# Performance work log

Hardware: AMD Instinct MI355X
Metric: run time of the kernel (lower is better)

The kernel has to match this reference:

```python
import jax, jax.numpy as jnp
import numpy as np

NEG_INF = -9e15


def setup_inputs() -> dict:
    key = jax.random.key(0)
    k1, k2, k3, k4 = jax.random.split(key, 4)
    N, F_in, H, F_out = 4096, 512, 8, 64
    node_features = jax.random.normal(k1, (N, F_in), dtype=jnp.float32)
    adj_matrix = jax.random.randint(k2, (N, N), 0, 2, dtype=jnp.int32)
    # ensure self-loops so every row has at least one unmasked entry
    adj_matrix = jnp.maximum(adj_matrix, jnp.eye(N, dtype=jnp.int32))
    W = jax.random.normal(k3, (H, F_in, F_out), dtype=jnp.float32) * 0.05
    a = jax.random.normal(k4, (H, 2 * F_out), dtype=jnp.float32) * 0.05
    return {"node_features": node_features, "adj_matrix": adj_matrix, "W": W, "a": a}


def reference(node_features, adj_matrix, W, a):
    alpha = 0.2
    H, F_in, F_out = W.shape
    # Per-head linear projection: [H, N, F_out]
    Wh = jnp.einsum("nf,hfo->hno", node_features, W)
    # Attention logits e_ij = LeakyReLU(a1 . Wh_i + a2 . Wh_j)
    f_src = jnp.einsum("hno,ho->hn", Wh, a[:, :F_out])   # [H, N]
    f_dst = jnp.einsum("hno,ho->hn", Wh, a[:, F_out:])   # [H, N]
    e = jax.nn.leaky_relu(f_src[:, :, None] + f_dst[:, None, :], negative_slope=alpha)  # [H, N, N]
    # Mask by adjacency, softmax over neighbors
    masked = jnp.where(adj_matrix[None, :, :] > 0, e, NEG_INF)
    attn = jax.nn.softmax(masked, axis=-1)               # [H, N, N]
    # Aggregate neighbor features per head
    h_prime = jnp.einsum("hnm,hmo->hno", attn, Wh)       # [H, N, F_out]
    # Concat heads along feature dim -> [N, H*F_out]
    return jnp.transpose(h_prime, (1, 0, 2)).reshape(h_prime.shape[1], H * F_out)
```

## Files before the change

kernel.cpp:

```cpp
#include <hip/hip_runtime.h>
#include <stdint.h>


#define NN 4096
#define FIN 512
#define NH 8
#define FO 64

typedef _Float16 f16x8 __attribute__((ext_vector_type(8)));
typedef _Float16 f16x2 __attribute__((ext_vector_type(2)));
typedef __attribute__((ext_vector_type(4))) float f32x4;

union H8 { f16x8 v; f16x2 p[4]; unsigned u[4]; };
union U2 { unsigned u; f16x2 v; };

#define GLOAD_LDS16(g, l)                                                          \
  __builtin_amdgcn_global_load_lds((__attribute__((address_space(1))) const void*)(g), \
                                   (__attribute__((address_space(3))) void*)(l), 16, 0, 0)
#define GLOAD_LDS4(g, l)                                                           \
  __builtin_amdgcn_global_load_lds((__attribute__((address_space(1))) const void*)(g), \
                                   (__attribute__((address_space(3))) void*)(l), 4, 0, 0)

__device__ __forceinline__ unsigned short f2h(float f) {
  _Float16 h = (_Float16)f;
  return __builtin_bit_cast(unsigned short, h);
}

__global__ __launch_bounds__(256) void prep_kernel(
    const float* __restrict__ X, const int* __restrict__ adj, const float* __restrict__ W,
    const float* __restrict__ a,
    unsigned short* __restrict__ Xh, unsigned short* __restrict__ WbT,
    unsigned* __restrict__ adjbitsT, unsigned short* __restrict__ WAh) {
  int bid = blockIdx.x, tid = threadIdx.x;
  if (bid < 2048) {
    int item = bid * 256 + tid;
    int jt = item >> 12, r = item & 4095;
    const int* p = adj + (size_t)r * NN + jt * 32;
    unsigned bits = 0;
#pragma unroll
    for (int b = 0; b < 32; b += 4) {
      int4 v = *(const int4*)(p + b);
      bits |= (unsigned)(v.x & 1) << b;
      bits |= (unsigned)(v.y & 1) << (b + 1);
      bits |= (unsigned)(v.z & 1) << (b + 2);
      bits |= (unsigned)(v.w & 1) << (b + 3);
    }
    adjbitsT[item] = bits;
  } else if (bid < 4096) {
    int item = (bid - 2048) * 256 + tid;
    float4 v = ((const float4*)X)[item];
    ushort4 o;
    o.x = f2h(v.x); o.y = f2h(v.y); o.z = f2h(v.z); o.w = f2h(v.w);
    ((ushort4*)Xh)[item] = o;
  } else if (bid < 5120) {
    int item = (bid - 4096) * 256 + tid;
    int o = item & 63, k = (item >> 6) & 511, h = item >> 15;
    WbT[h * 32768 + o * 512 + k] = f2h(W[h * 32768 + k * 64 + o]);
  } else {
    int item = (bid - 5120) * 256 + tid;
    int h = item >> 10, which = (item >> 9) & 1, k = item & 511;
    const float4* wp = (const float4*)(W + ((size_t)h * FIN + k) * FO);
    const float4* ap = (const float4*)(a + h * 128 + which * 64);
    float s = 0.f;
#pragma unroll
    for (int o4 = 0; o4 < 16; ++o4) {
      float4 w4 = wp[o4], a4 = ap[o4];
      s += w4.x * a4.x + w4.y * a4.y + w4.z * a4.z + w4.w * a4.w;
    }
    WAh[(h * 2 + which) * FIN + k] = f2h(s);
  }
}

__global__ __launch_bounds__(512, 4) void proj_sd_kernel(
    const unsigned short* __restrict__ Xh, const unsigned short* __restrict__ WbT,
    const unsigned short* __restrict__ WAh,
    unsigned short* __restrict__ Whfrag, float* __restrict__ Rf,
    unsigned short* __restrict__ E1h, unsigned short* __restrict__ E2h) {
  __shared__ float red[4 * 64 * 20];
  int lane = threadIdx.x & 63, wave = threadIdx.x >> 6;
  int row16 = lane & 15, grp = lane >> 4;
  int bx = blockIdx.x;
  if (bx >= 512) {
    int i0 = ((bx - 512) * 8 + wave) * 16;
    if (i0 >= NN) return;
    f32x4 acc = {0, 0, 0, 0};
    const unsigned short* xb = Xh + (size_t)(i0 + row16) * FIN + grp * 8;
    const unsigned short* wb = WAh + row16 * FIN + grp * 8;
#pragma unroll
    for (int k0 = 0; k0 < FIN; k0 += 32)
      acc = __builtin_amdgcn_mfma_f32_16x16x32_f16(*(const f16x8*)(xb + k0),
                                                   *(const f16x8*)(wb + k0), acc, 0, 0, 0);
    int hh = row16 >> 1;
#pragma unroll
    for (int reg = 0; reg < 4; ++reg) {
      int rr = i0 + grp * 4 + reg;
      float v = acc[reg];
      if (row16 & 1) {
        E1h[hh * NN + rr] = f2h(0.5f * __expf(v));
        E2h[hh * NN + rr] = f2h(0.5f * __expf(0.2f * v));
      } else {
        Rf[hh * NN + rr] = __expf(-0.8f * v);
      }
    }
    return;
  }
  int kh = wave >> 2, jb = wave & 3;
  int job = bx * 4 + jb;
  int h = job & 7, rt = job >> 3;
  int i0 = rt * 16;
  f32x4 acc[4] = {{0,0,0,0},{0,0,0,0},{0,0,0,0},{0,0,0,0}};
  const unsigned short* xb = Xh + (size_t)(i0 + row16) * FIN + kh * 256 + grp * 8;
  const unsigned short* wb = WbT + h * (FO * FIN) + row16 * FIN + kh * 256 + grp * 8;
#pragma unroll
  for (int k0 = 0; k0 < 256; k0 += 32) {
    f16x8 af = *(const f16x8*)(xb + k0);
#pragma unroll
    for (int cb = 0; cb < 4; ++cb)
      acc[cb] = __builtin_amdgcn_mfma_f32_16x16x32_f16(
          af, *(const f16x8*)(wb + cb * 16 * FIN + k0), acc[cb], 0, 0, 0);
  }
  if (kh == 1) {
    float* q = red + (jb * 64 + lane) * 20;
#pragma unroll
    for (int cb = 0; cb < 4; ++cb) *(f32x4*)(q + cb * 4) = acc[cb];
  }
  __syncthreads();
  if (kh == 0) {
    const float* q = red + (jb * 64 + lane) * 20;
#pragma unroll
    for (int cb = 0; cb < 4; ++cb) acc[cb] += *(const f32x4*)(q + cb * 4);
    int jt = i0 >> 5;
    int kk0 = (i0 & 31) + grp * 4;
    int tl = (kk0 >> 3) * 16 + row16;
    int e0 = kk0 & 7;
#pragma unroll
    for (int cb = 0; cb < 4; ++cb) {
      ushort4 pk;
      pk.x = f2h(acc[cb][0]); pk.y = f2h(acc[cb][1]);
      pk.z = f2h(acc[cb][2]); pk.w = f2h(acc[cb][3]);
      *(ushort4*)(Whfrag + (((size_t)h * 128 + jt) * 4 + cb) * 512 + tl * 8 + e0) = pk;
    }
  }
}

#define SEGB 4608
#define E_OFF 4096
#define A_OFF 4224

__global__ __launch_bounds__(256, 3) void gat_kernel(
    const unsigned* __restrict__ adjbitsT, const unsigned short* __restrict__ Whfrag,
    const float* __restrict__ Rf, const unsigned short* __restrict__ E1h,
    const unsigned short* __restrict__ E2h,
    float* __restrict__ N0, float* __restrict__ outbuf, float* __restrict__ Dd) {
  __shared__ __align__(16) char lds[36864];
  int h = blockIdx.y, z = blockIdx.z;
  int lane = threadIdx.x & 63, jseg = threadIdx.x >> 6;
  int row16 = lane & 15, grp = lane >> 4;
  int r0 = blockIdx.x * 64;
  int jt0 = z * 64 + jseg * 16;

  f16x2 Rh[4];
#pragma unroll
  for (int gi = 0; gi < 4; ++gi) {
    _Float16 rv = (_Float16)Rf[h * NN + r0 + gi * 16 + row16];
    Rh[gi][0] = rv; Rh[gi][1] = rv;
  }

  H8 ones;
#pragma unroll
  for (int k = 0; k < 4; ++k) ones.u[k] = 0x3C003C00u;

  const unsigned short* wsrc = Whfrag + (size_t)h * 262144 + (size_t)jt0 * 2048 + lane * 8;
  const unsigned short* esrc =
      ((lane & 4) ? E2h : E1h) + h * NN + jt0 * 32 + (lane & 3) * 8;
  const unsigned* asrc = adjbitsT + (size_t)jt0 * NN + r0 + lane;

  f32x4 acc[4][5];
#pragma unroll
  for (int gi = 0; gi < 4; ++gi)
#pragma unroll
    for (int cc = 0; cc < 5; ++cc) acc[gi][cc] = (f32x4){0, 0, 0, 0};

  char* seg0 = lds + (jseg * 2 + 0) * SEGB;
  char* seg1 = lds + (jseg * 2 + 1) * SEGB;

  auto stage = [&](char* seg, int p) {
    const unsigned short* bs = wsrc + (size_t)p * 2048;
    GLOAD_LDS16(bs, seg);
    GLOAD_LDS16(bs + 512, seg + 1024);
    GLOAD_LDS16(bs + 1024, seg + 2048);
    GLOAD_LDS16(bs + 1536, seg + 3072);
    GLOAD_LDS4(asrc + (size_t)p * NN, seg + A_OFF);
    if (lane < 8) GLOAD_LDS16(esrc + p * 32, seg + E_OFF);
  };

  auto compute = [&](const char* seg) {
    H8 e1, e2;
    e1.v = *(const f16x8*)(seg + E_OFF + grp * 16);
    e2.v = *(const f16x8*)(seg + E_OFF + 64 + grp * 16);
    const char* bp = seg + lane * 16;
    f16x8 b0 = *(const f16x8*)(bp);
    f16x8 b1 = *(const f16x8*)(bp + 1024);
    f16x8 b2 = *(const f16x8*)(bp + 2048);
    f16x8 b3 = *(const f16x8*)(bp + 3072);
#pragma unroll
    for (int gi = 0; gi < 4; ++gi) {
      unsigned bw = *(const unsigned*)(seg + A_OFF + (gi * 16 + row16) * 4);
      unsigned bb = (bw >> (grp * 8)) & 0xffu;
      unsigned t = bb | (bb << 15);
      H8 af;
#pragma unroll
      for (int k = 0; k < 4; ++k) {
        f16x2 mx = __builtin_elementwise_max(e1.p[k], Rh[gi] * e2.p[k]);
        U2 m;
        m.u = (t << (14 - 2 * k)) & 0x40004000u;
        af.p[k] = mx * m.v;
      }
      acc[gi][0] = __builtin_amdgcn_mfma_f32_16x16x32_f16(af.v, b0, acc[gi][0], 0, 0, 0);
      acc[gi][1] = __builtin_amdgcn_mfma_f32_16x16x32_f16(af.v, b1, acc[gi][1], 0, 0, 0);
      acc[gi][2] = __builtin_amdgcn_mfma_f32_16x16x32_f16(af.v, b2, acc[gi][2], 0, 0, 0);
      acc[gi][3] = __builtin_amdgcn_mfma_f32_16x16x32_f16(af.v, b3, acc[gi][3], 0, 0, 0);
      acc[gi][4] = __builtin_amdgcn_mfma_f32_16x16x32_f16(af.v, ones.v, acc[gi][4], 0, 0, 0);
    }
  };

  stage(seg0, 0);
  __syncthreads();
#pragma unroll 1
  for (int p2 = 0; p2 < 8; ++p2) {
    stage(seg1, 2 * p2 + 1);
    compute(seg0);
    __syncthreads();
    if (p2 < 7) stage(seg0, 2 * p2 + 2);
    compute(seg1);
    __syncthreads();
  }

  float* red = (float*)lds;
#pragma unroll
  for (int cc = 0; cc < 5; ++cc) {
    if (jseg != 0) {
#pragma unroll
      for (int gi = 0; gi < 4; ++gi)
        *(f32x4*)(red + (((jseg - 1) * 4 + gi) * 64 + lane) * 4) = acc[gi][cc];
    }
    __syncthreads();
    if (jseg == 0) {
#pragma unroll
      for (int s = 0; s < 3; ++s)
#pragma unroll
        for (int gi = 0; gi < 4; ++gi)
          acc[gi][cc] += *(const f32x4*)(red + ((s * 4 + gi) * 64 + lane) * 4);
    }
    __syncthreads();
  }

  if (jseg == 0) {
    float* base;
    int rs;
    if (z == 0) { base = N0 + (size_t)h * NN * FO; rs = FO; }
    else        { base = outbuf + h * FO;          rs = NH * FO; }
#pragma unroll
    for (int gi = 0; gi < 4; ++gi) {
#pragma unroll
      for (int reg = 0; reg < 4; ++reg) {
        int row = r0 + gi * 16 + grp * 4 + reg;
        float* op = base + (size_t)row * rs + row16;
        op[0]  = acc[gi][0][reg];
        op[16] = acc[gi][1][reg];
        op[32] = acc[gi][2][reg];
        op[48] = acc[gi][3][reg];
      }
      if (row16 == 0) {
#pragma unroll
        for (int reg = 0; reg < 4; ++reg)
          Dd[((size_t)z * NH + h) * NN + r0 + gi * 16 + grp * 4 + reg] = acc[gi][4][reg];
      }
    }
  }
}

__global__ __launch_bounds__(256) void norm_kernel(
    const float* __restrict__ N0, const float* __restrict__ Dd, float* __restrict__ out) {
  int idx = (blockIdx.x * 256 + threadIdx.x) * 4;
  int r = idx >> 9, c = idx & 511, h = c >> 6, o = c & 63;
  float4 n1 = *(const float4*)(out + idx);
  float4 n0 = *(const float4*)(N0 + ((size_t)h * NN + r) * FO + o);
  float inv = 1.0f / (Dd[h * NN + r] + Dd[(NH + h) * NN + r]);
  float4 res;
  res.x = (n1.x + n0.x) * inv;
  res.y = (n1.y + n0.y) * inv;
  res.z = (n1.z + n0.z) * inv;
  res.w = (n1.w + n0.w) * inv;
  *(float4*)(out + idx) = res;
}

extern "C" void kernel_launch(void* const* d_in, const int* in_sizes, int n_in,
                              void* d_out, int out_size, void* d_ws, size_t ws_size,
                              hipStream_t stream) {
  const float* X  = (const float*)d_in[0];
  const int* adj  = (const int*)d_in[1];
  const float* W  = (const float*)d_in[2];
  const float* a  = (const float*)d_in[3];
  float* out = (float*)d_out;
  char* ws = (char*)d_ws;

  unsigned short* Xh     = (unsigned short*)(ws + 0);
  unsigned short* WbT    = (unsigned short*)(ws + 4194304);
  unsigned* adjbitsT     = (unsigned*)(ws + 4718592);
  unsigned short* Whfrag = (unsigned short*)(ws + 6815744);
  unsigned short* WAh    = (unsigned short*)(ws + 11010048);
  float* Rf              = (float*)(ws + 11026432);
  unsigned short* E1h    = (unsigned short*)(ws + 11288576);
  unsigned short* E2h    = (unsigned short*)(ws + 11354112);
  float* N0              = (float*)(ws + 11534336);
  float* Dd              = (float*)(ws + 19922944);

  prep_kernel<<<5152, 256, 0, stream>>>(X, adj, W, a, Xh, WbT, adjbitsT, WAh);
  proj_sd_kernel<<<544, 512, 0, stream>>>(Xh, WbT, WAh, Whfrag, Rf, E1h, E2h);
  gat_kernel<<<dim3(64, 8, 2), 256, 0, stream>>>(adjbitsT, Whfrag, Rf, E1h, E2h, N0, out, Dd);
  norm_kernel<<<2048, 256, 0, stream>>>(N0, Dd, out);
}
```

Measured before the change: 86.80 us.

## Fuse X fp16 conversion into projection and drop split-K norm kernel

The separate X-to-fp16 pass in the prep kernel is removed; the projection kernel now loads fp32 X and converts it in registers. The attention kernel no longer splits the neighbor dimension across two z-blocks. Each block walks all 4096 columns and divides by the softmax denominator in its epilogue, which removes the N0/Dd intermediates and the norm kernel. The trade-off is half as many attention blocks (512 instead of 1024), so there is less parallelism and a longer serial loop per block, while X is read twice as fp32 by the projection.

Result: faster. 84.96 us (-2.1%).

```diff
diff --git a/kernel.cpp b/kernel.cpp
--- a/kernel.cpp
+++ b/kernel.cpp
@@ -26,11 +26,18 @@
   return __builtin_bit_cast(unsigned short, h);
 }
 
+__device__ __forceinline__ f16x8 ld_cvt8(const float* p) {
+  float4 a = *(const float4*)p, b = *(const float4*)(p + 4);
+  f16x8 r;
+  r[0] = (_Float16)a.x; r[1] = (_Float16)a.y; r[2] = (_Float16)a.z; r[3] = (_Float16)a.w;
+  r[4] = (_Float16)b.x; r[5] = (_Float16)b.y; r[6] = (_Float16)b.z; r[7] = (_Float16)b.w;
+  return r;
+}
+
 __global__ __launch_bounds__(256) void prep_kernel(
-    const float* __restrict__ X, const int* __restrict__ adj, const float* __restrict__ W,
-    const float* __restrict__ a,
-    unsigned short* __restrict__ Xh, unsigned short* __restrict__ WbT,
-    unsigned* __restrict__ adjbitsT, unsigned short* __restrict__ WAh) {
+    const int* __restrict__ adj, const float* __restrict__ W, const float* __restrict__ a,
+    unsigned short* __restrict__ WbT, unsigned* __restrict__ adjbitsT,
+    unsigned short* __restrict__ WAh) {
   int bid = blockIdx.x, tid = threadIdx.x;
   if (bid < 2048) {
     int item = bid * 256 + tid;
@@ -46,18 +53,12 @@
       bits |= (unsigned)(v.w & 1) << (b + 3);
     }
     adjbitsT[item] = bits;
-  } else if (bid < 4096) {
+  } else if (bid < 3072) {
     int item = (bid - 2048) * 256 + tid;
-    float4 v = ((const float4*)X)[item];
-    ushort4 o;
-    o.x = f2h(v.x); o.y = f2h(v.y); o.z = f2h(v.z); o.w = f2h(v.w);
-    ((ushort4*)Xh)[item] = o;
-  } else if (bid < 5120) {
-    int item = (bid - 4096) * 256 + tid;
     int o = item & 63, k = (item >> 6) & 511, h = item >> 15;
     WbT[h * 32768 + o * 512 + k] = f2h(W[h * 32768 + k * 64 + o]);
   } else {
-    int item = (bid - 5120) * 256 + tid;
+    int item = (bid - 3072) * 256 + tid;
     int h = item >> 10, which = (item >> 9) & 1, k = item & 511;
     const float4* wp = (const float4*)(W + ((size_t)h * FIN + k) * FO);
     const float4* ap = (const float4*)(a + h * 128 + which * 64);
@@ -72,7 +73,7 @@
 }
 
 __global__ __launch_bounds__(512, 4) void proj_sd_kernel(
-    const unsigned short* __restrict__ Xh, const unsigned short* __restrict__ WbT,
+    const float* __restrict__ X, const unsigned short* __restrict__ WbT,
     const unsigned short* __restrict__ WAh,
     unsigned short* __restrict__ Whfrag, float* __restrict__ Rf,
     unsigned short* __restrict__ E1h, unsigned short* __restrict__ E2h) {
@@ -84,11 +85,11 @@
     int i0 = ((bx - 512) * 8 + wave) * 16;
     if (i0 >= NN) return;
     f32x4 acc = {0, 0, 0, 0};
-    const unsigned short* xb = Xh + (size_t)(i0 + row16) * FIN + grp * 8;
+    const float* xb = X + (size_t)(i0 + row16) * FIN + grp * 8;
     const unsigned short* wb = WAh + row16 * FIN + grp * 8;
 #pragma unroll
     for (int k0 = 0; k0 < FIN; k0 += 32)
-      acc = __builtin_amdgcn_mfma_f32_16x16x32_f16(*(const f16x8*)(xb + k0),
+      acc = __builtin_amdgcn_mfma_f32_16x16x32_f16(ld_cvt8(xb + k0),
                                                    *(const f16x8*)(wb + k0), acc, 0, 0, 0);
     int hh = row16 >> 1;
 #pragma unroll
@@ -109,11 +110,11 @@
   int h = job & 7, rt = job >> 3;
   int i0 = rt * 16;
   f32x4 acc[4] = {{0,0,0,0},{0,0,0,0},{0,0,0,0},{0,0,0,0}};
-  const unsigned short* xb = Xh + (size_t)(i0 + row16) * FIN + kh * 256 + grp * 8;
+  const float* xb = X + (size_t)(i0 + row16) * FIN + kh * 256 + grp * 8;
   const unsigned short* wb = WbT + h * (FO * FIN) + row16 * FIN + kh * 256 + grp * 8;
 #pragma unroll
   for (int k0 = 0; k0 < 256; k0 += 32) {
-    f16x8 af = *(const f16x8*)(xb + k0);
+    f16x8 af = ld_cvt8(xb + k0);
 #pragma unroll
     for (int cb = 0; cb < 4; ++cb)
       acc[cb] = __builtin_amdgcn_mfma_f32_16x16x32_f16(
@@ -150,14 +151,13 @@
 __global__ __launch_bounds__(256, 3) void gat_kernel(
     const unsigned* __restrict__ adjbitsT, const unsigned short* __restrict__ Whfrag,
     const float* __restrict__ Rf, const unsigned short* __restrict__ E1h,
-    const unsigned short* __restrict__ E2h,
-    float* __restrict__ N0, float* __restrict__ outbuf, float* __restrict__ Dd) {
+    const unsigned short* __restrict__ E2h, float* __restrict__ out) {
   __shared__ __align__(16) char lds[36864];
-  int h = blockIdx.y, z = blockIdx.z;
+  int h = blockIdx.y;
   int lane = threadIdx.x & 63, jseg = threadIdx.x >> 6;
   int row16 = lane & 15, grp = lane >> 4;
   int r0 = blockIdx.x * 64;
-  int jt0 = z * 64 + jseg * 16;
+  int jt0 = jseg * 32;
 
   f16x2 Rh[4];
 #pragma unroll
@@ -227,11 +227,11 @@
   stage(seg0, 0);
   __syncthreads();
 #pragma unroll 1
-  for (int p2 = 0; p2 < 8; ++p2) {
+  for (int p2 = 0; p2 < 16; ++p2) {
     stage(seg1, 2 * p2 + 1);
     compute(seg0);
     __syncthreads();
-    if (p2 < 7) stage(seg0, 2 * p2 + 2);
+    if (p2 < 15) stage(seg0, 2 * p2 + 2);
     compute(seg1);
     __syncthreads();
   }
@@ -256,43 +256,20 @@
   }
 
   if (jseg == 0) {
-    float* base;
-    int rs;
-    if (z == 0) { base = N0 + (size_t)h * NN * FO; rs = FO; }
-    else        { base = outbuf + h * FO;          rs = NH * FO; }
 #pragma unroll
     for (int gi = 0; gi < 4; ++gi) {
 #pragma unroll
       for (int reg = 0; reg < 4; ++reg) {
+        float inv = 1.0f / acc[gi][4][reg];
         int row = r0 + gi * 16 + grp * 4 + reg;
-        float* op = base + (size_t)row * rs + row16;
-        op[0]  = acc[gi][0][reg];
-        op[16] = acc[gi][1][reg];
-        op[32] = acc[gi][2][reg];
-        op[48] = acc[gi][3][reg];
+        float* op = out + (size_t)row * (NH * FO) + h * FO + row16;
+        op[0]  = acc[gi][0][reg] * inv;
+        op[16] = acc[gi][1][reg] * inv;
+        op[32] = acc[gi][2][reg] * inv;
+        op[48] = acc[gi][3][reg] * inv;
       }
-      if (row16 == 0) {
-#pragma unroll
-        for (int reg = 0; reg < 4; ++reg)
-          Dd[((size_t)z * NH + h) * NN + r0 + gi * 16 + grp * 4 + reg] = acc[gi][4][reg];
-      }
-    }
-  }
-}
-
-__global__ __launch_bounds__(256) void norm_kernel(
-    const float* __restrict__ N0, const float* __restrict__ Dd, float* __restrict__ out) {
-  int idx = (blockIdx.x * 256 + threadIdx.x) * 4;
-  int r = idx >> 9, c = idx & 511, h = c >> 6, o = c & 63;
-  float4 n1 = *(const float4*)(out + idx);
-  float4 n0 = *(const float4*)(N0 + ((size_t)h * NN + r) * FO + o);
-  float inv = 1.0f / (Dd[h * NN + r] + Dd[(NH + h) * NN + r]);
-  float4 res;
-  res.x = (n1.x + n0.x) * inv;
-  res.y = (n1.y + n0.y) * inv;
-  res.z = (n1.z + n0.z) * inv;
-  res.w = (n1.w + n0.w) * inv;
-  *(float4*)(out + idx) = res;
+    }
+  }
 }
 
 extern "C" void kernel_launch(void* const* d_in, const int* in_sizes, int n_in,
@@ -305,19 +282,15 @@
   float* out = (float*)d_out;
   char* ws = (char*)d_ws;
 
-  unsigned short* Xh     = (unsigned short*)(ws + 0);
-  unsigned short* WbT    = (unsigned short*)(ws + 4194304);
-  unsigned* adjbitsT     = (unsigned*)(ws + 4718592);
-  unsigned short* Whfrag = (unsigned short*)(ws + 6815744);
-  unsigned short* WAh    = (unsigned short*)(ws + 11010048);
-  float* Rf              = (float*)(ws + 11026432);
-  unsigned short* E1h    = (unsigned short*)(ws + 11288576);
-  unsigned short* E2h    = (unsigned short*)(ws + 11354112);
-  float* N0              = (float*)(ws + 11534336);
-  float* Dd              = (float*)(ws + 19922944);
-
-  prep_kernel<<<5152, 256, 0, stream>>>(X, adj, W, a, Xh, WbT, adjbitsT, WAh);
-  proj_sd_kernel<<<544, 512, 0, stream>>>(Xh, WbT, WAh, Whfrag, Rf, E1h, E2h);
-  gat_kernel<<<dim3(64, 8, 2), 256, 0, stream>>>(adjbitsT, Whfrag, Rf, E1h, E2h, N0, out, Dd);
-  norm_kernel<<<2048, 256, 0, stream>>>(N0, Dd, out);
-}
+  unsigned short* WbT    = (unsigned short*)(ws + 0);
+  unsigned* adjbitsT     = (unsigned*)(ws + 524288);
+  unsigned short* Whfrag = (unsigned short*)(ws + 2621440);
+  unsigned short* WAh    = (unsigned short*)(ws + 6815744);
+  float* Rf              = (float*)(ws + 6832128);
+  unsigned short* E1h    = (unsigned short*)(ws + 6963200);
+  unsigned short* E2h    = (unsigned short*)(ws + 7028736);
+
+  prep_kernel<<<3104, 256, 0, stream>>>(adj, W, a, WbT, adjbitsT, WAh);
+  proj_sd_kernel<<<544, 512, 0, stream>>>(X, WbT, WAh, Whfrag, Rf, E1h, E2h);
+  gat_kernel<<<dim3(64, 8), 256, 0, stream>>>(adjbitsT, Whfrag, Rf, E1h, E2h, out);
+}
```

## Register-prefetch GAT tiles, drop z-split and fuse normalization into gat kernel

Applied to the files above, without the earlier changes.

Replaces the LDS-staged global_load_lds double buffer in the attention kernel with direct global loads into a register-held Tile, double-buffered in registers with no block barriers inside the main loop. The z split over neighbor halves is removed: each wave now covers 32 tiles, so the grid halves to 512 blocks. The softmax normalization is done in the epilogue, which removes the separate norm_kernel and the N0/Dd partial buffers. This saves a launch and the partial-result traffic, at the cost of fewer blocks, lower occupancy (launch bound 2), more register pressure and a longer serial loop per wave.

After: 77.90 us. -10.3%, faster.

```diff
diff --git a/kernel.cpp b/kernel.cpp
--- a/kernel.cpp
+++ b/kernel.cpp
@@ -13,13 +13,6 @@
 
 union H8 { f16x8 v; f16x2 p[4]; unsigned u[4]; };
 union U2 { unsigned u; f16x2 v; };
-
-#define GLOAD_LDS16(g, l)                                                          \
-  __builtin_amdgcn_global_load_lds((__attribute__((address_space(1))) const void*)(g), \
-                                   (__attribute__((address_space(3))) void*)(l), 16, 0, 0)
-#define GLOAD_LDS4(g, l)                                                           \
-  __builtin_amdgcn_global_load_lds((__attribute__((address_space(1))) const void*)(g), \
-                                   (__attribute__((address_space(3))) void*)(l), 4, 0, 0)
 
 __device__ __forceinline__ unsigned short f2h(float f) {
   _Float16 h = (_Float16)f;
@@ -143,21 +136,22 @@
   }
 }
 
-#define SEGB 4608
-#define E_OFF 4096
-#define A_OFF 4224
-
-__global__ __launch_bounds__(256, 3) void gat_kernel(
+struct Tile {
+  f16x8 b0, b1, b2, b3;
+  f16x8 e1, e2;
+  unsigned aw0, aw1, aw2, aw3;
+};
+
+__global__ __launch_bounds__(256, 2) void gat_kernel(
     const unsigned* __restrict__ adjbitsT, const unsigned short* __restrict__ Whfrag,
     const float* __restrict__ Rf, const unsigned short* __restrict__ E1h,
-    const unsigned short* __restrict__ E2h,
-    float* __restrict__ N0, float* __restrict__ outbuf, float* __restrict__ Dd) {
-  __shared__ __align__(16) char lds[36864];
-  int h = blockIdx.y, z = blockIdx.z;
+    const unsigned short* __restrict__ E2h, float* __restrict__ out) {
+  __shared__ __align__(16) float red[3072];
+  int h = blockIdx.y;
   int lane = threadIdx.x & 63, jseg = threadIdx.x >> 6;
   int row16 = lane & 15, grp = lane >> 4;
   int r0 = blockIdx.x * 64;
-  int jt0 = z * 64 + jseg * 16;
+  int jt0 = jseg * 32;
 
   f16x2 Rh[4];
 #pragma unroll
@@ -171,9 +165,9 @@
   for (int k = 0; k < 4; ++k) ones.u[k] = 0x3C003C00u;
 
   const unsigned short* wsrc = Whfrag + (size_t)h * 262144 + (size_t)jt0 * 2048 + lane * 8;
-  const unsigned short* esrc =
-      ((lane & 4) ? E2h : E1h) + h * NN + jt0 * 32 + (lane & 3) * 8;
-  const unsigned* asrc = adjbitsT + (size_t)jt0 * NN + r0 + lane;
+  const unsigned short* e1p = E1h + h * NN + jt0 * 32 + grp * 8;
+  const unsigned short* e2p = E2h + h * NN + jt0 * 32 + grp * 8;
+  const unsigned* ap = adjbitsT + (size_t)jt0 * NN + r0 + row16;
 
   f32x4 acc[4][5];
 #pragma unroll
@@ -181,62 +175,58 @@
 #pragma unroll
     for (int cc = 0; cc < 5; ++cc) acc[gi][cc] = (f32x4){0, 0, 0, 0};
 
-  char* seg0 = lds + (jseg * 2 + 0) * SEGB;
-  char* seg1 = lds + (jseg * 2 + 1) * SEGB;
-
-  auto stage = [&](char* seg, int p) {
+  auto ld = [&](int p, Tile& t) {
     const unsigned short* bs = wsrc + (size_t)p * 2048;
-    GLOAD_LDS16(bs, seg);
-    GLOAD_LDS16(bs + 512, seg + 1024);
-    GLOAD_LDS16(bs + 1024, seg + 2048);
-    GLOAD_LDS16(bs + 1536, seg + 3072);
-    GLOAD_LDS4(asrc + (size_t)p * NN, seg + A_OFF);
-    if (lane < 8) GLOAD_LDS16(esrc + p * 32, seg + E_OFF);
+    t.b0 = *(const f16x8*)(bs);
+    t.b1 = *(const f16x8*)(bs + 512);
+    t.b2 = *(const f16x8*)(bs + 1024);
+    t.b3 = *(const f16x8*)(bs + 1536);
+    t.e1 = *(const f16x8*)(e1p + p * 32);
+    t.e2 = *(const f16x8*)(e2p + p * 32);
+    const unsigned* aq = ap + (size_t)p * NN;
+    t.aw0 = aq[0]; t.aw1 = aq[16]; t.aw2 = aq[32]; t.aw3 = aq[48];
   };
 
-  auto compute = [&](const char* seg) {
+  auto compute = [&](const Tile& t) {
     H8 e1, e2;
-    e1.v = *(const f16x8*)(seg + E_OFF + grp * 16);
-    e2.v = *(const f16x8*)(seg + E_OFF + 64 + grp * 16);
-    const char* bp = seg + lane * 16;
-    f16x8 b0 = *(const f16x8*)(bp);
-    f16x8 b1 = *(const f16x8*)(bp + 1024);
-    f16x8 b2 = *(const f16x8*)(bp + 2048);
-    f16x8 b3 = *(const f16x8*)(bp + 3072);
+    e1.v = t.e1; e2.v = t.e2;
+    unsigned aw[4] = {t.aw0, t.aw1, t.aw2, t.aw3};
 #pragma unroll
     for (int gi = 0; gi < 4; ++gi) {
-      unsigned bw = *(const unsigned*)(seg + A_OFF + (gi * 16 + row16) * 4);
-      unsigned bb = (bw >> (grp * 8)) & 0xffu;
-      unsigned t = bb | (bb << 15);
+      unsigned bb = (aw[gi] >> (grp * 8)) & 0xffu;
+      unsigned tt = bb | (bb << 15);
       H8 af;
 #pragma unroll
       for (int k = 0; k < 4; ++k) {
         f16x2 mx = __builtin_elementwise_max(e1.p[k], Rh[gi] * e2.p[k]);
         U2 m;
-        m.u = (t << (14 - 2 * k)) & 0x40004000u;
+        m.u = (tt << (14 - 2 * k)) & 0x40004000u;
         af.p[k] = mx * m.v;
       }
-      acc[gi][0] = __builtin_amdgcn_mfma_f32_16x16x32_f16(af.v, b0, acc[gi][0], 0, 0, 0);
-      acc[gi][1] = __builtin_amdgcn_mfma_f32_16x16x32_f16(af.v, b1, acc[gi][1], 0, 0, 0);
-      acc[gi][2] = __builtin_amdgcn_mfma_f32_16x16x32_f16(af.v, b2, acc[gi][2], 0, 0, 0);
-      acc[gi][3] = __builtin_amdgcn_mfma_f32_16x16x32_f16(af.v, b3, acc[gi][3], 0, 0, 0);
+      acc[gi][0] = __builtin_amdgcn_mfma_f32_16x16x32_f16(af.v, t.b0, acc[gi][0], 0, 0, 0);
+      acc[gi][1] = __builtin_amdgcn_mfma_f32_16x16x32_f16(af.v, t.b1, acc[gi][1], 0, 0, 0);
+      acc[gi][2] = __builtin_amdgcn_mfma_f32_16x16x32_f16(af.v, t.b2, acc[gi][2], 0, 0, 0);
+      acc[gi][3] = __builtin_amdgcn_mfma_f32_16x16x32_f16(af.v, t.b3, acc[gi][3], 0, 0, 0);
       acc[gi][4] = __builtin_amdgcn_mfma_f32_16x16x32_f16(af.v, ones.v, acc[gi][4], 0, 0, 0);
     }
   };
 
-  stage(seg0, 0);
+  Tile tA, tB;
+  ld(0, tA);
+#pragma unroll 1
+  for (int p2 = 0; p2 < 15; ++p2) {
+    ld(2 * p2 + 1, tB);
+    asm volatile("" ::: "memory");
+    compute(tA);
+    ld(2 * p2 + 2, tA);
+    asm volatile("" ::: "memory");
+    compute(tB);
+  }
+  ld(31, tB);
+  compute(tA);
+  compute(tB);
+
   __syncthreads();
-#pragma unroll 1
-  for (int p2 = 0; p2 < 8; ++p2) {
-    stage(seg1, 2 * p2 + 1);
-    compute(seg0);
-    __syncthreads();
-    if (p2 < 7) stage(seg0, 2 * p2 + 2);
-    compute(seg1);
-    __syncthreads();
-  }
-
-  float* red = (float*)lds;
 #pragma unroll
   for (int cc = 0; cc < 5; ++cc) {
     if (jseg != 0) {
@@ -256,43 +246,20 @@
   }
 
   if (jseg == 0) {
-    float* base;
-    int rs;
-    if (z == 0) { base = N0 + (size_t)h * NN * FO; rs = FO; }
-    else        { base = outbuf + h * FO;          rs = NH * FO; }
 #pragma unroll
     for (int gi = 0; gi < 4; ++gi) {
 #pragma unroll
       for (int reg = 0; reg < 4; ++reg) {
+        float inv = 1.0f / acc[gi][4][reg];
         int row = r0 + gi * 16 + grp * 4 + reg;
-        float* op = base + (size_t)row * rs + row16;
-        op[0]  = acc[gi][0][reg];
-        op[16] = acc[gi][1][reg];
-        op[32] = acc[gi][2][reg];
-        op[48] = acc[gi][3][reg];
+        float* op = out + (size_t)row * (NH * FO) + h * FO + row16;
+        op[0]  = acc[gi][0][reg] * inv;
+        op[16] = acc[gi][1][reg] * inv;
+        op[32] = acc[gi][2][reg] * inv;
+        op[48] = acc[gi][3][reg] * inv;
       }
-      if (row16 == 0) {
-#pragma unroll
-        for (int reg = 0; reg < 4; ++reg)
-          Dd[((size_t)z * NH + h) * NN + r0 + gi * 16 + grp * 4 + reg] = acc[gi][4][reg];
-      }
-    }
-  }
-}
-
-__global__ __launch_bounds__(256) void norm_kernel(
-    const float* __restrict__ N0, const float* __restrict__ Dd, float* __restrict__ out) {
-  int idx = (blockIdx.x * 256 + threadIdx.x) * 4;
-  int r = idx >> 9, c = idx & 511, h = c >> 6, o = c & 63;
-  float4 n1 = *(const float4*)(out + idx);
-  float4 n0 = *(const float4*)(N0 + ((size_t)h * NN + r) * FO + o);
-  float inv = 1.0f / (Dd[h * NN + r] + Dd[(NH + h) * NN + r]);
-  float4 res;
-  res.x = (n1.x + n0.x) * inv;
-  res.y = (n1.y + n0.y) * inv;
-  res.z = (n1.z + n0.z) * inv;
-  res.w = (n1.w + n0.w) * inv;
-  *(float4*)(out + idx) = res;
+    }
+  }
 }
 
 extern "C" void kernel_launch(void* const* d_in, const int* in_sizes, int n_in,
@@ -313,11 +280,8 @@
   float* Rf              = (float*)(ws + 11026432);
   unsigned short* E1h    = (unsigned short*)(ws + 11288576);
   unsigned short* E2h    = (unsigned short*)(ws + 11354112);
-  float* N0              = (float*)(ws + 11534336);
-  float* Dd              = (float*)(ws + 19922944);
 
   prep_kernel<<<5152, 256, 0, stream>>>(X, adj, W, a, Xh, WbT, adjbitsT, WAh);
   proj_sd_kernel<<<544, 512, 0, stream>>>(Xh, WbT, WAh, Whfrag, Rf, E1h, E2h);
-  gat_kernel<<<dim3(64, 8, 2), 256, 0, stream>>>(adjbitsT, Whfrag, Rf, E1h, E2h, N0, out, Dd);
-  norm_kernel<<<2048, 256, 0, stream>>>(N0, Dd, out);
-}
+  gat_kernel<<<dim3(64, 8), 256, 0, stream>>>(adjbitsT, Whfrag, Rf, E1h, E2h, out);
+}
```
